# Kernel tuning notes

Hardware: AMD Instinct MI355X
Metric: run time of the kernel (lower is better)

Reference implementation:

```python
import jax, jax.numpy as jnp
import numpy as np

N_HEADS = 16
HEAD_DIM = 64
ROPE_BASE = 10000.0
EPS = 1e-6


def _rope_tables(T, hd, dtype):
    inv_freq = 1.0 / (ROPE_BASE ** (jnp.arange(0, hd, 2, dtype=jnp.float32) / hd))
    freqs = jnp.arange(T, dtype=jnp.float32)[:, None] * inv_freq[None, :]  # [T, hd/2]
    cos = jnp.cos(freqs)[None, :, None, :].astype(dtype)  # [1,T,1,hd/2]
    sin = jnp.sin(freqs)[None, :, None, :].astype(dtype)
    return cos, sin


def _apply_rope(x, cos, sin):
    d = x.shape[-1] // 2
    x1, x2 = x[..., :d], x[..., d:]
    return jnp.concatenate([x1 * cos + x2 * sin, -x1 * sin + x2 * cos], axis=-1)


def setup_inputs() -> dict:
    key = jax.random.key(0)
    k1, k2, k3, k4 = jax.random.split(key, 4)
    B, T, C = 4, 1024, 1024
    x = jax.random.normal(k1, (B, T, C), dtype=jnp.float32)
    W_qkv = jax.random.normal(k2, (3 * C, C), dtype=jnp.float32) * (1.0 / np.sqrt(C))
    W_out = jax.random.normal(k3, (C, C), dtype=jnp.float32) * (1.0 / np.sqrt(C))
    # learnable per-head curvature, init = exp(randn) * base_curvature (base=1.0)
    hyp_k = jnp.exp(jax.random.normal(k4, (1, N_HEADS, 1, 1), dtype=jnp.float32))
    return {"x": x, "W_qkv": W_qkv, "W_out": W_out, "hyp_k": hyp_k}


def reference(x, W_qkv, W_out, hyp_k):
    B, T, C = x.shape
    H, hd = N_HEADS, HEAD_DIM
    qkv = x @ W_qkv.T  # [B,T,3C]
    q, k, v = jnp.split(qkv, 3, axis=-1)
    q = q.reshape(B, T, H, hd)
    k = k.reshape(B, T, H, hd)
    v = v.reshape(B, T, H, hd)

    cos, sin = _rope_tables(T, hd, x.dtype)
    q = _apply_rope(q, cos, sin)
    k = _apply_rope(k, cos, sin)

    # [B,H,T,hd]
    q = q.transpose(0, 2, 1, 3)
    k = k.transpose(0, 2, 1, 3)
    v = v.transpose(0, 2, 1, 3)

    # Lorentz lift: x0 = sqrt(k + ||x||^2); inner = -x0*y0 + <x,y>;
    # dist = sqrt(k) * arccosh(-inner / k)  (geoopt Lorentz convention)
    kc = hyp_k[:, :, :, 0]  # [1,H,1]
    q0 = jnp.sqrt(kc + jnp.sum(q * q, axis=-1))  # [B,H,T]
    k0 = jnp.sqrt(kc + jnp.sum(k * k, axis=-1))  # [B,H,T]
    inner = jnp.einsum('bhld,bhsd->bhls', q, k) - q0[..., None] * k0[:, :, None, :]
    arg = jnp.maximum(-inner / hyp_k, 1.0 + EPS)
    dis = jnp.sqrt(hyp_k) * jnp.arccosh(arg)  # [B,H,L,S]

    attn_weight = 1.0 / (EPS + dis)
    causal = jnp.tril(jnp.ones((T, T), dtype=bool))
    attn_weight = jnp.where(causal, attn_weight, -jnp.inf)
    attn = jax.nn.softmax(attn_weight, axis=-1)
    out = jnp.einsum('bhls,bhsd->bhld', attn, v)  # [B,H,T,hd]
    out = out.transpose(0, 2, 1, 3).reshape(B, T, C)
    return out @ W_out.T
```

## Files before the change

kernel.cpp:

```cpp
#include <hip/hip_runtime.h>

#define B_ 4
#define T_ 1024
#define C_ 1024
#define H_ 16
#define HD_ 64

typedef short bf16x8 __attribute__((ext_vector_type(8)));
typedef float f32x4 __attribute__((ext_vector_type(4)));

__device__ __forceinline__ ushort f2bf(float f) {
    union { float f; unsigned u; } v; v.f = f;
    unsigned u = v.u;
    unsigned r = (u + 0x7fffu + ((u >> 16) & 1u)) >> 16;
    return (ushort)r;
}

__device__ __forceinline__ f32x4 mfma16(bf16x8 a, bf16x8 b, f32x4 c) {
    return __builtin_amdgcn_mfma_f32_16x16x32_bf16(a, b, c, 0, 0, 0);
}

__device__ __forceinline__ bf16x8 lds_frag(const ushort* base, int row, int byteoff) {
    int addr = (row * 128 + byteoff) ^ ((row & 7) << 4);
    uint4 u = *(const uint4*)((const char*)base + addr);
    return __builtin_bit_cast(bf16x8, u);
}

__device__ __forceinline__ bf16x8 lds_frag_v(const ushort* base, int d, int byteoff) {
    int addr = (d * 128 + byteoff) ^ ((((d & 7) ^ (d >> 3)) & 7) << 4);
    uint4 u = *(const uint4*)((const char*)base + addr);
    return __builtin_bit_cast(bf16x8, u);
}

__device__ __forceinline__ bf16x8 lds_frag_p(const ushort* base, int row, int byteoff) {
    int addr = (row * 128 + byteoff) ^ (((row >> 2) & 3) << 5);
    uint4 u = *(const uint4*)((const char*)base + addr);
    return __builtin_bit_cast(bf16x8, u);
}

__device__ __forceinline__ void bar_lds() {
    asm volatile("s_waitcnt lgkmcnt(0)" ::: "memory");
    __builtin_amdgcn_sched_barrier(0);
    __builtin_amdgcn_s_barrier();
    __builtin_amdgcn_sched_barrier(0);
}

__global__ void cast_all(const float* __restrict__ x, const float* __restrict__ wqkv,
                         const float* __restrict__ wout,
                         ushort* __restrict__ xb, ushort* __restrict__ wqkvb,
                         ushort* __restrict__ woutb) {
    int i = (blockIdx.x * 256 + threadIdx.x) * 4;
    const float* src; ushort* dst; int off;
    if (i < 4194304)      { src = x;    dst = xb;    off = i; }
    else if (i < 7340032) { src = wqkv; dst = wqkvb; off = i - 4194304; }
    else                  { src = wout; dst = woutb; off = i - 7340032; }
    float4 v = *(const float4*)(src + off);
    ushort4 o = make_ushort4(f2bf(v.x), f2bf(v.y), f2bf(v.z), f2bf(v.w));
    *(ushort4*)(dst + off) = o;
}


#define GEMM_COMPUTE_128x64(As, Bs)                                                       \
    {                                                                                     \
        _Pragma("unroll")                                                                 \
        for (int ks = 0; ks < 2; ++ks) {                                                  \
            bf16x8 af[2], bfr[4];                                                         \
            _Pragma("unroll")                                                             \
            for (int mf = 0; mf < 2; ++mf)                                                \
                af[mf] = lds_frag(As, wv * 32 + mf * 16 + (lane & 15),                    \
                                  ks * 64 + ((lane >> 4) << 4));                          \
            _Pragma("unroll")                                                             \
            for (int nf = 0; nf < 4; ++nf)                                                \
                bfr[nf] = lds_frag(Bs, nf * 16 + (lane & 15),                             \
                                   ks * 64 + ((lane >> 4) << 4));                         \
            _Pragma("unroll")                                                             \
            for (int mf = 0; mf < 2; ++mf)                                                \
                _Pragma("unroll")                                                         \
                for (int nf = 0; nf < 4; ++nf)                                            \
                    acc[mf][nf] = mfma16(af[mf], bfr[nf], acc[mf][nf]);                   \
        }                                                                                 \
    }

#define GEMM_DBUF_STAGING(Asrc, Bsrc)                                                     \
    const int srow = tid >> 3, soff = (tid & 7) * 8;                                      \
    const int swz = (srow & 7) << 4;                                                      \
    uint4 a0, a1, a2, a3, b0, b1;                                                         \
    auto issue = [&](int kt) {                                                            \
        const ushort* Ap = Asrc + kt * 64;                                                \
        const ushort* Bp = Bsrc + kt * 64;                                                \
        a0 = *(const uint4*)(Ap + (size_t)srow * C_ + soff);                              \
        a1 = *(const uint4*)(Ap + (size_t)(32 + srow) * C_ + soff);                       \
        a2 = *(const uint4*)(Ap + (size_t)(64 + srow) * C_ + soff);                       \
        a3 = *(const uint4*)(Ap + (size_t)(96 + srow) * C_ + soff);                       \
        b0 = *(const uint4*)(Bp + (size_t)srow * C_ + soff);                              \
        b1 = *(const uint4*)(Bp + (size_t)(32 + srow) * C_ + soff);                       \
    };                                                                                    \
    auto lwrite = [&](ushort* Ad, ushort* Bd) {                                           \
        *(uint4*)((char*)Ad + ((tid * 16) ^ swz)) = a0;                                   \
        *(uint4*)((char*)Ad + (((tid + 256) * 16) ^ swz)) = a1;                           \
        *(uint4*)((char*)Ad + (((tid + 512) * 16) ^ swz)) = a2;                           \
        *(uint4*)((char*)Ad + (((tid + 768) * 16) ^ swz)) = a3;                           \
        *(uint4*)((char*)Bd + ((tid * 16) ^ swz)) = b0;                                   \
        *(uint4*)((char*)Bd + (((tid + 256) * 16) ^ swz)) = b1;                           \
    }

#define GEMM_DBUF_LOOP(COMPUTE)                                                           \
    issue(0);                                                                             \
    lwrite(As0, Bs0);                                                                     \
    issue(1);                                                                             \
    bar_lds();                                                                            \
    for (int kt = 0; kt < 12; kt += 2) {                                                  \
        lwrite(As1, Bs1);                                                                 \
        issue(kt + 2);                                                                    \
        COMPUTE(As0, Bs0);                                                                \
        bar_lds();                                                                        \
        lwrite(As0, Bs0);                                                                 \
        issue(kt + 3);                                                                    \
        COMPUTE(As1, Bs1);                                                                \
        bar_lds();                                                                        \
    }                                                                                     \
    lwrite(As1, Bs1);                                                                     \
    issue(14);                                                                            \
    COMPUTE(As0, Bs0);                                                                    \
    bar_lds();                                                                            \
    lwrite(As0, Bs0);                                                                     \
    issue(15);                                                                            \
    COMPUTE(As1, Bs1);                                                                    \
    bar_lds();                                                                            \
    lwrite(As1, Bs1);                                                                     \
    COMPUTE(As0, Bs0);                                                                    \
    bar_lds();                                                                            \
    COMPUTE(As1, Bs1);

#define GEMM_COMPUTE_128x128(As, Bs)                                                      \
    {                                                                                     \
        _Pragma("unroll")                                                                 \
        for (int ks = 0; ks < 2; ++ks) {                                                  \
            bf16x8 af[4], bfr[4];                                                         \
            _Pragma("unroll")                                                             \
            for (int mf = 0; mf < 4; ++mf)                                                \
                af[mf] = lds_frag(As, wr * 64 + mf * 16 + (lane & 15),                    \
                                  ks * 64 + ((lane >> 4) << 4));                          \
            _Pragma("unroll")                                                             \
            for (int nf = 0; nf < 4; ++nf)                                                \
                bfr[nf] = lds_frag(Bs, wc * 64 + nf * 16 + (lane & 15),                   \
                                   ks * 64 + ((lane >> 4) << 4));                         \
            _Pragma("unroll")                                                             \
            for (int mf = 0; mf < 4; ++mf)                                                \
                _Pragma("unroll")                                                         \
                for (int nf = 0; nf < 4; ++nf)                                            \
                    acc[mf][nf] = mfma16(af[mf], bfr[nf], acc[mf][nf]);                   \
        }                                                                                 \
    }

#define GEMM_DBUF_STAGING2(Asrc, Bsrc)                                                    \
    const int srow = tid >> 3, soff = (tid & 7) * 8;                                      \
    const int swz = (srow & 7) << 4;                                                      \
    uint4 a0, a1, a2, a3, b0, b1, b2, b3;                                                 \
    auto issue = [&](int kt) {                                                            \
        const ushort* Ap = Asrc + kt * 64;                                                \
        const ushort* Bp = Bsrc + kt * 64;                                                \
        a0 = *(const uint4*)(Ap + (size_t)srow * C_ + soff);                              \
        a1 = *(const uint4*)(Ap + (size_t)(32 + srow) * C_ + soff);                       \
        a2 = *(const uint4*)(Ap + (size_t)(64 + srow) * C_ + soff);                       \
        a3 = *(const uint4*)(Ap + (size_t)(96 + srow) * C_ + soff);                       \
        b0 = *(const uint4*)(Bp + (size_t)srow * C_ + soff);                              \
        b1 = *(const uint4*)(Bp + (size_t)(32 + srow) * C_ + soff);                       \
        b2 = *(const uint4*)(Bp + (size_t)(64 + srow) * C_ + soff);                       \
        b3 = *(const uint4*)(Bp + (size_t)(96 + srow) * C_ + soff);                       \
    };                                                                                    \
    auto lwrite = [&](ushort* Ad, ushort* Bd) {                                           \
        *(uint4*)((char*)Ad + ((tid * 16) ^ swz)) = a0;                                   \
        *(uint4*)((char*)Ad + (((tid + 256) * 16) ^ swz)) = a1;                           \
        *(uint4*)((char*)Ad + (((tid + 512) * 16) ^ swz)) = a2;                           \
        *(uint4*)((char*)Ad + (((tid + 768) * 16) ^ swz)) = a3;                           \
        *(uint4*)((char*)Bd + ((tid * 16) ^ swz)) = b0;                                   \
        *(uint4*)((char*)Bd + (((tid + 256) * 16) ^ swz)) = b1;                           \
        *(uint4*)((char*)Bd + (((tid + 512) * 16) ^ swz)) = b2;                           \
        *(uint4*)((char*)Bd + (((tid + 768) * 16) ^ swz)) = b3;                           \
    }

__global__ __launch_bounds__(256) void gemm_qkv(
    const ushort* __restrict__ Xb, const ushort* __restrict__ Wb,
    const float* __restrict__ hyp,
    ushort* __restrict__ Qo, ushort* __restrict__ Ko, ushort* __restrict__ Vo,
    float* __restrict__ q0g, float* __restrict__ k0g)
{
    __shared__ ushort As0[128 * 64], Bs0[128 * 64];
    __shared__ ushort As1[128 * 64], Bs1[128 * 64];
    const int tid = threadIdx.x, lane = tid & 63, wv = tid >> 6;
    const int wr = wv >> 1, wc = wv & 1;
    const int m0 = blockIdx.x * 128, n0 = blockIdx.y * 128;
    const ushort* Asrc = Xb + (size_t)m0 * C_;
    const ushort* Bsrc = Wb + (size_t)n0 * C_;

    GEMM_DBUF_STAGING2(Asrc, Bsrc);

    f32x4 acc[4][4] = {};
    GEMM_DBUF_LOOP(GEMM_COMPUTE_128x128);

    const int sector = n0 >> 10;
    const int h = ((n0 & 1023) >> 6) + wc;
    const float kc = hyp[h];
    const float inv_k = 1.0f / kc;
    float invf[2];
    invf[0] = __expf(-0.28782313662425572f * (float)(lane & 15));
    invf[1] = __expf(-0.28782313662425572f * (float)(16 + (lane & 15)));

#pragma unroll
    for (int mf = 0; mf < 4; ++mf) {
        float o[4][4];
#pragma unroll
        for (int nf = 0; nf < 4; ++nf)
#pragma unroll
            for (int r = 0; r < 4; ++r) o[nf][r] = acc[mf][nf][r];

        if (sector < 2) {
#pragma unroll
            for (int p = 0; p < 2; ++p) {
#pragma unroll
                for (int r = 0; r < 4; ++r) {
                    int m = m0 + wr * 64 + mf * 16 + ((lane >> 4) << 2) + r;
                    int t = m & (T_ - 1);
                    float sn, cs; __sincosf((float)t * invf[p], &sn, &cs);
                    float x1 = o[p][r], x2 = o[p + 2][r];
                    o[p][r]     =  x1 * cs + x2 * sn;
                    o[p + 2][r] = -x1 * sn + x2 * cs;
                }
            }
        }

#pragma unroll
        for (int r = 0; r < 4; ++r) {
            int m = m0 + wr * 64 + mf * 16 + ((lane >> 4) << 2) + r;
            int b = m >> 10, t = m & (T_ - 1);
            int bh = b * H_ + h;
            size_t base = ((size_t)bh * T_ + t) * HD_;
            float nrm = 0.f;
#pragma unroll
            for (int nf = 0; nf < 4; ++nf) {
                int d = nf * 16 + (lane & 15);
                float v = o[nf][r];
                nrm += v * v;
                ushort bv = f2bf(sector == 1 ? v * inv_k : v);
                if (sector == 0)      Qo[base + d] = bv;
                else if (sector == 1) Ko[base + d] = bv;
                else                  Vo[base + d] = bv;
            }
            if (sector < 2) {
#pragma unroll
                for (int mk = 1; mk < 16; mk <<= 1) nrm += __shfl_xor(nrm, mk);
                if ((lane & 15) == 0) {
                    float v0 = sqrtf(kc + nrm);
                    if (sector == 0) q0g[(size_t)bh * T_ + t] = v0;
                    else             k0g[(size_t)bh * T_ + t] = v0 * inv_k;
                }
            }
        }
    }
}

__global__ __launch_bounds__(256, 2) void attn_fwd(
    const ushort* __restrict__ Q, const ushort* __restrict__ K, const ushort* __restrict__ V,
    const float* __restrict__ q0g, const float* __restrict__ k0g,
    const float* __restrict__ hyp, ushort* __restrict__ AO)
{
    __shared__ ushort Ks[64 * 64];
    __shared__ ushort Vts[64 * 64];
    __shared__ ushort Ps[4][16 * 64];
    __shared__ float k0s[64];

    const int tid = threadIdx.x, lane = tid & 63, wv = tid >> 6;
    const int pr = blockIdx.x >> 6;
    const int bh = blockIdx.x & 63;
    const int h = bh & (H_ - 1);
    const int qa = pr, qb = 15 - pr, nt = qb + 1;
    const float c3 = sqrtf(hyp[h]) * 0.48045301391820142f;
    const float e3 = 6.931471805599453e-07f;

    const ushort* Kb = K + (size_t)bh * T_ * HD_;
    const ushort* Vb = V + (size_t)bh * T_ * HD_;

    bf16x8 aqA[2], aqB[2];
    {
        const ushort* qA = Q + ((size_t)bh * T_ + qa * 64 + wv * 16 + (lane & 15)) * HD_;
        const ushort* qB = Q + ((size_t)bh * T_ + qb * 64 + wv * 16 + (lane & 15)) * HD_;
#pragma unroll
        for (int ks = 0; ks < 2; ++ks) {
            aqA[ks] = __builtin_bit_cast(bf16x8, *(const uint4*)(qA + ks * 32 + ((lane >> 4) << 3)));
            aqB[ks] = __builtin_bit_cast(bf16x8, *(const uint4*)(qB + ks * 32 + ((lane >> 4) << 3)));
        }
    }
    float q0A[4], q0B[4];
#pragma unroll
    for (int r = 0; r < 4; ++r) {
        int rr = wv * 16 + ((lane >> 4) << 2) + r;
        q0A[r] = q0g[(size_t)bh * T_ + qa * 64 + rr];
        q0B[r] = q0g[(size_t)bh * T_ + qb * 64 + rr];
    }

    f32x4 oaccA[4] = {}, oaccB[4] = {};
    float lpA[4] = {}, lpB[4] = {};

    const int krow = tid >> 3, koff = tid & 7;
    const int sp = tid >> 3, dc = tid & 7;
    uint4 kv0, kv1, vv0, vv1;
    float kz = 0.f;
    auto issue = [&](int s0) {
        kv0 = *(const uint4*)(Kb + (size_t)(s0 + krow) * HD_ + koff * 8);
        kv1 = *(const uint4*)(Kb + (size_t)(s0 + 32 + krow) * HD_ + koff * 8);
        vv0 = *(const uint4*)(Vb + (size_t)(s0 + 2 * sp) * HD_ + dc * 8);
        vv1 = *(const uint4*)(Vb + (size_t)(s0 + 2 * sp + 1) * HD_ + dc * 8);
        if (tid < 64) kz = k0g[(size_t)bh * T_ + s0 + tid];
    };

    auto geom = [&](const f32x4* sc, const float* q0, const float* k0r, float p[4][4]) {
#pragma unroll
        for (int r = 0; r < 4; ++r)
#pragma unroll
            for (int sf = 0; sf < 4; ++sf) {
                float arg = fmaf(q0[r], k0r[sf], -sc[sf][r]);
                arg = fmaxf(arg, 1.0f + 1e-6f);
                float t = fmaf(arg, arg, -1.0f);
                float u = arg + __builtin_amdgcn_sqrtf(t);
                float l2 = __builtin_amdgcn_logf(u);
                float w2 = fmaf(l2, c3, e3);
                float rv = fminf(__builtin_amdgcn_rcpf(w2), 30.0f);
                p[sf][r] = __builtin_amdgcn_exp2f(rv);
            }
    };
    auto mask_diag = [&](float p[4][4]) {
        const int qloc = wv * 16 + ((lane >> 4) << 2);
#pragma unroll
        for (int r = 0; r < 4; ++r)
#pragma unroll
            for (int sf = 0; sf < 4; ++sf)
                if (sf * 16 + (lane & 15) > qloc + r) p[sf][r] = 0.f;
    };
    auto pv_step = [&](float p[4][4], ushort* ps, const bf16x8 (&vf)[2][4],
                       f32x4* oacc, float* lp) {
#pragma unroll
        for (int r = 0; r < 4; ++r) {
            int row = ((lane >> 4) << 2) + r;
#pragma unroll
            for (int sf = 0; sf < 4; ++sf) {
                int addr = (row * 128 + (sf * 16 + (lane & 15)) * 2) ^ (((row >> 2) & 3) << 5);
                *(ushort*)((char*)ps + addr) = f2bf(p[sf][r]);
            }
            lp[r] += (p[0][r] + p[1][r]) + (p[2][r] + p[3][r]);
        }
#pragma unroll
        for (int ks = 0; ks < 2; ++ks) {
            bf16x8 ap = lds_frag_p(ps, lane & 15, ks * 64 + ((lane >> 4) << 4));
#pragma unroll
            for (int df = 0; df < 4; ++df)
                oacc[df] = mfma16(ap, vf[ks][df], oacc[df]);
        }
    };

    issue(0);

    for (int it = 0; it < nt; ++it) {
        const bool actA = (it <= qa);
        __syncthreads();
        {
            *(uint4*)((char*)Ks + ((tid * 16) ^ ((krow & 7) << 4))) = kv0;
            int c1 = tid + 256;
            *(uint4*)((char*)Ks + ((c1 * 16) ^ (((c1 >> 3) & 7) << 4))) = kv1;
            union { uint4 v; ushort u[8]; } a, b;
            a.v = vv0; b.v = vv1;
#pragma unroll
            for (int j = 0; j < 8; ++j) {
                int d = dc * 8 + j;
                uint pack = (uint)a.u[j] | ((uint)b.u[j] << 16);
                *(uint*)((char*)Vts + ((d * 128 + sp * 4) ^ (((j ^ dc) & 7) << 4))) = pack;
            }
            if (tid < 64) k0s[tid] = kz;
        }
        if (it + 1 < nt) issue((it + 1) * 64);
        __syncthreads();

        bf16x8 bk[2][4];
#pragma unroll
        for (int ks = 0; ks < 2; ++ks)
#pragma unroll
            for (int sf = 0; sf < 4; ++sf)
                bk[ks][sf] = lds_frag(Ks, sf * 16 + (lane & 15), ks * 64 + ((lane >> 4) << 4));

        float k0r[4];
#pragma unroll
        for (int sf = 0; sf < 4; ++sf) k0r[sf] = k0s[sf * 16 + (lane & 15)];

        f32x4 scB[4] = {};
#pragma unroll
        for (int ks = 0; ks < 2; ++ks)
#pragma unroll
            for (int sf = 0; sf < 4; ++sf)
                scB[sf] = mfma16(aqB[ks], bk[ks][sf], scB[sf]);
        f32x4 scA[4] = {};
        if (actA) {
#pragma unroll
            for (int ks = 0; ks < 2; ++ks)
#pragma unroll
                for (int sf = 0; sf < 4; ++sf)
                    scA[sf] = mfma16(aqA[ks], bk[ks][sf], scA[sf]);
        }

        bf16x8 vf[2][4];
#pragma unroll
        for (int ks = 0; ks < 2; ++ks)
#pragma unroll
            for (int df = 0; df < 4; ++df)
                vf[ks][df] = lds_frag_v(Vts, df * 16 + (lane & 15), ks * 64 + ((lane >> 4) << 4));

        float pB[4][4];
        geom(scB, q0B, k0r, pB);
        if (it == qb) mask_diag(pB);
        pv_step(pB, Ps[wv], vf, oaccB, lpB);

        if (actA) {
            float pA[4][4];
            geom(scA, q0A, k0r, pA);
            if (it == qa) mask_diag(pA);
            pv_step(pA, Ps[wv], vf, oaccA, lpA);
        }
    }

    const int b = bh >> 4;
    auto epi = [&](f32x4* oacc, float* lp, int qt) {
#pragma unroll
        for (int r = 0; r < 4; ++r) {
            float s = lp[r];
#pragma unroll
            for (int mk = 1; mk < 16; mk <<= 1) s += __shfl_xor(s, mk);
            float invl = __builtin_amdgcn_rcpf(s);
            int t = qt * 64 + wv * 16 + ((lane >> 4) << 2) + r;
            size_t base = ((size_t)b * T_ + t) * C_ + h * HD_;
#pragma unroll
            for (int df = 0; df < 4; ++df)
                AO[base + df * 16 + (lane & 15)] = f2bf(oacc[df][r] * invl);
        }
    };
    epi(oaccA, lpA, qa);
    epi(oaccB, lpB, qb);
}

__global__ __launch_bounds__(256) void gemm_out(
    const ushort* __restrict__ Ab, const ushort* __restrict__ Wb, float* __restrict__ Out)
{
    __shared__ ushort As0[128 * 64], Bs0[64 * 64];
    __shared__ ushort As1[128 * 64], Bs1[64 * 64];
    const int tid = threadIdx.x, lane = tid & 63, wv = tid >> 6;
    const int m0 = blockIdx.x * 128, n0 = blockIdx.y * 64;
    const ushort* Asrc = Ab + (size_t)m0 * C_;
    const ushort* Bsrc = Wb + (size_t)n0 * C_;

    GEMM_DBUF_STAGING(Asrc, Bsrc);

    f32x4 acc[2][4] = {};
    GEMM_DBUF_LOOP(GEMM_COMPUTE_128x64);

#pragma unroll
    for (int mf = 0; mf < 2; ++mf)
#pragma unroll
        for (int r = 0; r < 4; ++r) {
            int m = m0 + wv * 32 + mf * 16 + ((lane >> 4) << 2) + r;
#pragma unroll
            for (int nf = 0; nf < 4; ++nf) {
                int n = n0 + nf * 16 + (lane & 15);
                Out[(size_t)m * C_ + n] = acc[mf][nf][r];
            }
        }
}

extern "C" void kernel_launch(void* const* d_in, const int* in_sizes, int n_in,
                              void* d_out, int out_size, void* d_ws, size_t ws_size,
                              hipStream_t stream)
{
    const float* x    = (const float*)d_in[0];
    const float* wqkv = (const float*)d_in[1];
    const float* wout = (const float*)d_in[2];
    const float* hyp  = (const float*)d_in[3];

    char* ws = (char*)d_ws;
    ushort* xb    = (ushort*)(ws + 0);
    ushort* wqkvb = (ushort*)(ws + 8388608);
    ushort* woutb = (ushort*)(ws + 14680064);
    ushort* Qb    = (ushort*)(ws + 16777216);
    ushort* Kb    = (ushort*)(ws + 25165824);
    ushort* Vb    = (ushort*)(ws + 33554432);
    ushort* Ab    = (ushort*)(ws + 41943040);
    float*  q0    = (float*)(ws + 50331648);
    float*  k0    = (float*)(ws + 50593792);

    cast_all<<<8192, 256, 0, stream>>>(x, wqkv, wout, xb, wqkvb, woutb);

    gemm_qkv<<<dim3(32, 24), 256, 0, stream>>>(xb, wqkvb, hyp, Qb, Kb, Vb, q0, k0);
    attn_fwd<<<512, 256, 0, stream>>>(Qb, Kb, Vb, q0, k0, hyp, Ab);
    gemm_out<<<dim3(32, 16), 256, 0, stream>>>(Ab, woutb, (float*)d_out);
}
```

Before: 93.74 us.

## Stage QKV GEMM tiles with direct global-to-LDS loads and vmcnt barriers

The QKV projection GEMM now uses global_load_lds (direct global-to-shared DMA) to fill its double-buffered A and B tiles. This replaces the register-staged load followed by an LDS write. The pipeline waits on vmcnt(8) so the next tile's loads stay in flight while the current tile is computed, and the XOR swizzle is applied on the global address side instead. This removes VGPR staging and LDS store instructions. The risk is synchronization hazards and a changed bank-conflict pattern. gemm_out is only moved in the file and keeps its old staging.

Measured after the change: 95.63 us. +2.0%, slower.

```diff
diff --git a/kernel.cpp b/kernel.cpp
--- a/kernel.cpp
+++ b/kernel.cpp
@@ -43,6 +43,36 @@
     __builtin_amdgcn_sched_barrier(0);
     __builtin_amdgcn_s_barrier();
     __builtin_amdgcn_sched_barrier(0);
+}
+__device__ __forceinline__ void bar_plain() {
+    __builtin_amdgcn_sched_barrier(0);
+    __builtin_amdgcn_s_barrier();
+    __builtin_amdgcn_sched_barrier(0);
+}
+__device__ __forceinline__ void bar_vm8() {
+    asm volatile("s_waitcnt vmcnt(8)" ::: "memory");
+    __builtin_amdgcn_sched_barrier(0);
+    __builtin_amdgcn_s_barrier();
+    __builtin_amdgcn_sched_barrier(0);
+}
+__device__ __forceinline__ void bar_vm0() {
+    asm volatile("s_waitcnt vmcnt(0)" ::: "memory");
+    __builtin_amdgcn_sched_barrier(0);
+    __builtin_amdgcn_s_barrier();
+    __builtin_amdgcn_sched_barrier(0);
+}
+
+__device__ __forceinline__ void stage128(ushort* sbase, const ushort* gtile, int wv, int lane) {
+    const int srow = lane >> 3;
+    const ushort* g0 = gtile + (size_t)srow * C_ + ((((lane & 7) ^ srow)) << 3);
+#pragma unroll
+    for (int i = 0; i < 4; ++i) {
+        int w = wv * 4 + i;
+        const ushort* g = g0 + (size_t)(w * 8) * C_;
+        ushort* l = sbase + w * 512;
+        __builtin_amdgcn_global_load_lds((const __attribute__((address_space(1))) void*)g,
+                                         (__attribute__((address_space(3))) void*)l, 16, 0, 0);
+    }
 }
 
 __global__ void cast_all(const float* __restrict__ x, const float* __restrict__ wqkv,
@@ -58,79 +88,6 @@
     ushort4 o = make_ushort4(f2bf(v.x), f2bf(v.y), f2bf(v.z), f2bf(v.w));
     *(ushort4*)(dst + off) = o;
 }
-
-
-#define GEMM_COMPUTE_128x64(As, Bs)                                                       \
-    {                                                                                     \
-        _Pragma("unroll")                                                                 \
-        for (int ks = 0; ks < 2; ++ks) {                                                  \
-            bf16x8 af[2], bfr[4];                                                         \
-            _Pragma("unroll")                                                             \
-            for (int mf = 0; mf < 2; ++mf)                                                \
-                af[mf] = lds_frag(As, wv * 32 + mf * 16 + (lane & 15),                    \
-                                  ks * 64 + ((lane >> 4) << 4));                          \
-            _Pragma("unroll")                                                             \
-            for (int nf = 0; nf < 4; ++nf)                                                \
-                bfr[nf] = lds_frag(Bs, nf * 16 + (lane & 15),                             \
-                                   ks * 64 + ((lane >> 4) << 4));                         \
-            _Pragma("unroll")                                                             \
-            for (int mf = 0; mf < 2; ++mf)                                                \
-                _Pragma("unroll")                                                         \
-                for (int nf = 0; nf < 4; ++nf)                                            \
-                    acc[mf][nf] = mfma16(af[mf], bfr[nf], acc[mf][nf]);                   \
-        }                                                                                 \
-    }
-
-#define GEMM_DBUF_STAGING(Asrc, Bsrc)                                                     \
-    const int srow = tid >> 3, soff = (tid & 7) * 8;                                      \
-    const int swz = (srow & 7) << 4;                                                      \
-    uint4 a0, a1, a2, a3, b0, b1;                                                         \
-    auto issue = [&](int kt) {                                                            \
-        const ushort* Ap = Asrc + kt * 64;                                                \
-        const ushort* Bp = Bsrc + kt * 64;                                                \
-        a0 = *(const uint4*)(Ap + (size_t)srow * C_ + soff);                              \
-        a1 = *(const uint4*)(Ap + (size_t)(32 + srow) * C_ + soff);                       \
-        a2 = *(const uint4*)(Ap + (size_t)(64 + srow) * C_ + soff);                       \
-        a3 = *(const uint4*)(Ap + (size_t)(96 + srow) * C_ + soff);                       \
-        b0 = *(const uint4*)(Bp + (size_t)srow * C_ + soff);                              \
-        b1 = *(const uint4*)(Bp + (size_t)(32 + srow) * C_ + soff);                       \
-    };                                                                                    \
-    auto lwrite = [&](ushort* Ad, ushort* Bd) {                                           \
-        *(uint4*)((char*)Ad + ((tid * 16) ^ swz)) = a0;                                   \
-        *(uint4*)((char*)Ad + (((tid + 256) * 16) ^ swz)) = a1;                           \
-        *(uint4*)((char*)Ad + (((tid + 512) * 16) ^ swz)) = a2;                           \
-        *(uint4*)((char*)Ad + (((tid + 768) * 16) ^ swz)) = a3;                           \
-        *(uint4*)((char*)Bd + ((tid * 16) ^ swz)) = b0;                                   \
-        *(uint4*)((char*)Bd + (((tid + 256) * 16) ^ swz)) = b1;                           \
-    }
-
-#define GEMM_DBUF_LOOP(COMPUTE)                                                           \
-    issue(0);                                                                             \
-    lwrite(As0, Bs0);                                                                     \
-    issue(1);                                                                             \
-    bar_lds();                                                                            \
-    for (int kt = 0; kt < 12; kt += 2) {                                                  \
-        lwrite(As1, Bs1);                                                                 \
-        issue(kt + 2);                                                                    \
-        COMPUTE(As0, Bs0);                                                                \
-        bar_lds();                                                                        \
-        lwrite(As0, Bs0);                                                                 \
-        issue(kt + 3);                                                                    \
-        COMPUTE(As1, Bs1);                                                                \
-        bar_lds();                                                                        \
-    }                                                                                     \
-    lwrite(As1, Bs1);                                                                     \
-    issue(14);                                                                            \
-    COMPUTE(As0, Bs0);                                                                    \
-    bar_lds();                                                                            \
-    lwrite(As0, Bs0);                                                                     \
-    issue(15);                                                                            \
-    COMPUTE(As1, Bs1);                                                                    \
-    bar_lds();                                                                            \
-    lwrite(As1, Bs1);                                                                     \
-    COMPUTE(As0, Bs0);                                                                    \
-    bar_lds();                                                                            \
-    COMPUTE(As1, Bs1);
 
 #define GEMM_COMPUTE_128x128(As, Bs)                                                      \
     {                                                                                     \
@@ -153,33 +110,6 @@
         }                                                                                 \
     }
 
-#define GEMM_DBUF_STAGING2(Asrc, Bsrc)                                                    \
-    const int srow = tid >> 3, soff = (tid & 7) * 8;                                      \
-    const int swz = (srow & 7) << 4;                                                      \
-    uint4 a0, a1, a2, a3, b0, b1, b2, b3;                                                 \
-    auto issue = [&](int kt) {                                                            \
-        const ushort* Ap = Asrc + kt * 64;                                                \
-        const ushort* Bp = Bsrc + kt * 64;                                                \
-        a0 = *(const uint4*)(Ap + (size_t)srow * C_ + soff);                              \
-        a1 = *(const uint4*)(Ap + (size_t)(32 + srow) * C_ + soff);                       \
-        a2 = *(const uint4*)(Ap + (size_t)(64 + srow) * C_ + soff);                       \
-        a3 = *(const uint4*)(Ap + (size_t)(96 + srow) * C_ + soff);                       \
-        b0 = *(const uint4*)(Bp + (size_t)srow * C_ + soff);                              \
-        b1 = *(const uint4*)(Bp + (size_t)(32 + srow) * C_ + soff);                       \
-        b2 = *(const uint4*)(Bp + (size_t)(64 + srow) * C_ + soff);                       \
-        b3 = *(const uint4*)(Bp + (size_t)(96 + srow) * C_ + soff);                       \
-    };                                                                                    \
-    auto lwrite = [&](ushort* Ad, ushort* Bd) {                                           \
-        *(uint4*)((char*)Ad + ((tid * 16) ^ swz)) = a0;                                   \
-        *(uint4*)((char*)Ad + (((tid + 256) * 16) ^ swz)) = a1;                           \
-        *(uint4*)((char*)Ad + (((tid + 512) * 16) ^ swz)) = a2;                           \
-        *(uint4*)((char*)Ad + (((tid + 768) * 16) ^ swz)) = a3;                           \
-        *(uint4*)((char*)Bd + ((tid * 16) ^ swz)) = b0;                                   \
-        *(uint4*)((char*)Bd + (((tid + 256) * 16) ^ swz)) = b1;                           \
-        *(uint4*)((char*)Bd + (((tid + 512) * 16) ^ swz)) = b2;                           \
-        *(uint4*)((char*)Bd + (((tid + 768) * 16) ^ swz)) = b3;                           \
-    }
-
 __global__ __launch_bounds__(256) void gemm_qkv(
     const ushort* __restrict__ Xb, const ushort* __restrict__ Wb,
     const float* __restrict__ hyp,
@@ -194,10 +124,29 @@
     const ushort* Asrc = Xb + (size_t)m0 * C_;
     const ushort* Bsrc = Wb + (size_t)n0 * C_;
 
-    GEMM_DBUF_STAGING2(Asrc, Bsrc);
+    auto stage = [&](ushort* Ad, ushort* Bd, int kt) {
+        stage128(Ad, Asrc + kt * 64, wv, lane);
+        stage128(Bd, Bsrc + kt * 64, wv, lane);
+    };
+
+    stage(As0, Bs0, 0);
+    stage(As1, Bs1, 1);
 
     f32x4 acc[4][4] = {};
-    GEMM_DBUF_LOOP(GEMM_COMPUTE_128x128);
+    for (int kt = 0; kt < 14; kt += 2) {
+        bar_vm8();
+        GEMM_COMPUTE_128x128(As0, Bs0);
+        bar_plain();
+        stage(As0, Bs0, kt + 2);
+        bar_vm8();
+        GEMM_COMPUTE_128x128(As1, Bs1);
+        bar_plain();
+        stage(As1, Bs1, kt + 3);
+    }
+    bar_vm8();
+    GEMM_COMPUTE_128x128(As0, Bs0);
+    bar_vm0();
+    GEMM_COMPUTE_128x128(As1, Bs1);
 
     const int sector = n0 >> 10;
     const int h = ((n0 & 1023) >> 6) + wc;
@@ -258,6 +207,100 @@
             }
         }
     }
+}
+
+#define GEMM_COMPUTE_128x64(As, Bs)                                                       \
+    {                                                                                     \
+        _Pragma("unroll")                                                                 \
+        for (int ks = 0; ks < 2; ++ks) {                                                  \
+            bf16x8 af[2], bfr[4];                                                         \
+            _Pragma("unroll")                                                             \
+            for (int mf = 0; mf < 2; ++mf)                                                \
+                af[mf] = lds_frag(As, wv * 32 + mf * 16 + (lane & 15),                    \
+                                  ks * 64 + ((lane >> 4) << 4));                          \
+            _Pragma("unroll")                                                             \
+            for (int nf = 0; nf < 4; ++nf)                                                \
+                bfr[nf] = lds_frag(Bs, nf * 16 + (lane & 15),                             \
+                                   ks * 64 + ((lane >> 4) << 4));                        \
+            _Pragma("unroll")                                                             \
+            for (int mf = 0; mf < 2; ++mf)                                                \
+                _Pragma("unroll")                                                         \
+                for (int nf = 0; nf < 4; ++nf)                                            \
+                    acc[mf][nf] = mfma16(af[mf], bfr[nf], acc[mf][nf]);                   \
+        }                                                                                 \
+    }
+
+__global__ __launch_bounds__(256) void gemm_out(
+    const ushort* __restrict__ Ab, const ushort* __restrict__ Wb, float* __restrict__ Out)
+{
+    __shared__ ushort As0[128 * 64], Bs0[64 * 64];
+    __shared__ ushort As1[128 * 64], Bs1[64 * 64];
+    const int tid = threadIdx.x, lane = tid & 63, wv = tid >> 6;
+    const int m0 = blockIdx.x * 128, n0 = blockIdx.y * 64;
+    const ushort* Asrc = Ab + (size_t)m0 * C_;
+    const ushort* Bsrc = Wb + (size_t)n0 * C_;
+
+    const int srow = tid >> 3, soff = (tid & 7) * 8;
+    const int swz = (srow & 7) << 4;
+    uint4 a0, a1, a2, a3, b0, b1;
+    auto issue = [&](int kt) {
+        const ushort* Ap = Asrc + kt * 64;
+        const ushort* Bp = Bsrc + kt * 64;
+        a0 = *(const uint4*)(Ap + (size_t)srow * C_ + soff);
+        a1 = *(const uint4*)(Ap + (size_t)(32 + srow) * C_ + soff);
+        a2 = *(const uint4*)(Ap + (size_t)(64 + srow) * C_ + soff);
+        a3 = *(const uint4*)(Ap + (size_t)(96 + srow) * C_ + soff);
+        b0 = *(const uint4*)(Bp + (size_t)srow * C_ + soff);
+        b1 = *(const uint4*)(Bp + (size_t)(32 + srow) * C_ + soff);
+    };
+    auto lwrite = [&](ushort* Ad, ushort* Bd) {
+        *(uint4*)((char*)Ad + ((tid * 16) ^ swz)) = a0;
+        *(uint4*)((char*)Ad + (((tid + 256) * 16) ^ swz)) = a1;
+        *(uint4*)((char*)Ad + (((tid + 512) * 16) ^ swz)) = a2;
+        *(uint4*)((char*)Ad + (((tid + 768) * 16) ^ swz)) = a3;
+        *(uint4*)((char*)Bd + ((tid * 16) ^ swz)) = b0;
+        *(uint4*)((char*)Bd + (((tid + 256) * 16) ^ swz)) = b1;
+    };
+
+    f32x4 acc[2][4] = {};
+    issue(0);
+    lwrite(As0, Bs0);
+    issue(1);
+    bar_lds();
+    for (int kt = 0; kt < 12; kt += 2) {
+        lwrite(As1, Bs1);
+        issue(kt + 2);
+        GEMM_COMPUTE_128x64(As0, Bs0);
+        bar_lds();
+        lwrite(As0, Bs0);
+        issue(kt + 3);
+        GEMM_COMPUTE_128x64(As1, Bs1);
+        bar_lds();
+    }
+    lwrite(As1, Bs1);
+    issue(14);
+    GEMM_COMPUTE_128x64(As0, Bs0);
+    bar_lds();
+    lwrite(As0, Bs0);
+    issue(15);
+    GEMM_COMPUTE_128x64(As1, Bs1);
+    bar_lds();
+    lwrite(As1, Bs1);
+    GEMM_COMPUTE_128x64(As0, Bs0);
+    bar_lds();
+    GEMM_COMPUTE_128x64(As1, Bs1);
+
+#pragma unroll
+    for (int mf = 0; mf < 2; ++mf)
+#pragma unroll
+        for (int r = 0; r < 4; ++r) {
+            int m = m0 + wv * 32 + mf * 16 + ((lane >> 4) << 2) + r;
+#pragma unroll
+            for (int nf = 0; nf < 4; ++nf) {
+                int n = n0 + nf * 16 + (lane & 15);
+                Out[(size_t)m * C_ + n] = acc[mf][nf][r];
+            }
+        }
 }
 
 __global__ __launch_bounds__(256, 2) void attn_fwd(
@@ -445,34 +488,6 @@
     epi(oaccB, lpB, qb);
 }
 
-__global__ __launch_bounds__(256) void gemm_out(
-    const ushort* __restrict__ Ab, const ushort* __restrict__ Wb, float* __restrict__ Out)
-{
-    __shared__ ushort As0[128 * 64], Bs0[64 * 64];
-    __shared__ ushort As1[128 * 64], Bs1[64 * 64];
-    const int tid = threadIdx.x, lane = tid & 63, wv = tid >> 6;
-    const int m0 = blockIdx.x * 128, n0 = blockIdx.y * 64;
-    const ushort* Asrc = Ab + (size_t)m0 * C_;
-    const ushort* Bsrc = Wb + (size_t)n0 * C_;
-
-    GEMM_DBUF_STAGING(Asrc, Bsrc);
-
-    f32x4 acc[2][4] = {};
-    GEMM_DBUF_LOOP(GEMM_COMPUTE_128x64);
-
-#pragma unroll
-    for (int mf = 0; mf < 2; ++mf)
-#pragma unroll
-        for (int r = 0; r < 4; ++r) {
-            int m = m0 + wv * 32 + mf * 16 + ((lane >> 4) << 2) + r;
-#pragma unroll
-            for (int nf = 0; nf < 4; ++nf) {
-                int n = n0 + nf * 16 + (lane & 15);
-                Out[(size_t)m * C_ + n] = acc[mf][nf][r];
-            }
-        }
-}
-
 extern "C" void kernel_launch(void* const* d_in, const int* in_sizes, int n_in,
                               void* d_out, int out_size, void* d_ws, size_t ws_size,
                               hipStream_t stream)
```
